# Kernel optimization log

Measured on AMD Instinct MI355X. Metric: run time of the kernel, lower is better.

Reference implementation:

```python
import jax, jax.numpy as jnp
import numpy as np

B, C, H, W = 32, 256, 64, 64
h, w = 8, 8          # partition size
S = 4                # num_sharesets
RED = 4              # globalperceptron_reduce
EPS = 1e-5           # BatchNorm eps


def setup_inputs() -> dict:
    key = jax.random.key(0)
    ks = jax.random.split(key, 20)
    Ci = C // RED
    def bn_params(i):
        return (1.0 + 0.1 * jax.random.normal(ks[i], (S,), jnp.float32),      # gamma
                0.1 * jax.random.normal(ks[i + 1], (S,), jnp.float32),        # beta
                0.1 * jax.random.normal(ks[i + 2], (S,), jnp.float32),        # running_mean
                jax.random.uniform(ks[i + 3], (S,), jnp.float32, 0.5, 1.5))   # running_var
    g3, b3, m3, v3 = bn_params(6)
    g1, b1, m1, v1 = bn_params(10)
    gk, bk, mk, vk = bn_params(14)
    return {
        "x": jax.random.normal(ks[0], (B, C, H, W), jnp.float32),
        # GlobalPerceptron (1x1 convs on pooled vector == dense layers)
        "fc1_w": 0.05 * jax.random.normal(ks[1], (Ci, C), jnp.float32),
        "fc1_b": jnp.zeros((Ci,), jnp.float32),
        "fc2_w": 0.05 * jax.random.normal(ks[2], (C, Ci), jnp.float32),
        "fc2_b": jnp.zeros((C,), jnp.float32),
        # fc3: grouped 1x1 conv over S*h*w channels -> S independent (h*w,h*w) mats
        "fc3_w": 0.05 * jax.random.normal(ks[3], (S, h * w, h * w), jnp.float32),
        "fc3bn_g": g3, "fc3bn_b": b3, "fc3bn_m": m3, "fc3bn_v": v3,
        # reparam depthwise conv branches (k=1 and k=3), groups=S
        "conv1_w": 0.1 * jax.random.normal(ks[4], (S, 1, 1, 1), jnp.float32),
        "bn1_g": g1, "bn1_b": b1, "bn1_m": m1, "bn1_v": v1,
        "conv3_w": 0.1 * jax.random.normal(ks[5], (S, 1, 3, 3), jnp.float32),
        "bn3_g": gk, "bn3_b": bk, "bn3_m": mk, "bn3_v": vk,
    }


def _bn(x, g, b, m, v):
    # inference-mode BatchNorm2d over channel dim 1 (S channels)
    scale = g / jnp.sqrt(v + EPS)
    return x * scale[None, :, None, None] + (b - m * scale)[None, :, None, None]


def _dwconv(x, wgt, k):
    # depthwise (groups=S) conv, stride 1, SAME-ish padding k//2
    return jax.lax.conv_general_dilated(
        x, wgt, (1, 1), [(k // 2, k // 2)] * 2,
        feature_group_count=S, dimension_numbers=("NCHW", "OIHW", "NCHW"))


def reference(x, fc1_w, fc1_b, fc2_w, fc2_b, fc3_w,
              fc3bn_g, fc3bn_b, fc3bn_m, fc3bn_v,
              conv1_w, bn1_g, bn1_b, bn1_m, bn1_v,
              conv3_w, bn3_g, bn3_b, bn3_m, bn3_v):
    hp, wp = H // h, W // w
    # GlobalPerceptron gate: avgpool -> fc -> relu -> fc -> sigmoid
    pooled = x.mean((2, 3))  # (B, C)
    gate = jax.nn.sigmoid(jnp.maximum(pooled @ fc1_w.T + fc1_b, 0.0) @ fc2_w.T + fc2_b)
    # partition: (B,C,H,W) -> (B,hp,wp,C,h,w)
    parts = x.reshape(B, C, hp, h, wp, w).transpose(0, 2, 4, 1, 3, 5)
    # fc3 grouped 1x1 conv: rows of S consecutive channels' (h*w) patches
    fc_in = parts.reshape(-1, S, h * w)                      # (B*hp*wp*C/S, S, h*w)
    fc3_out = jnp.einsum('nsi,soi->nso', fc_in, fc3_w).reshape(-1, S, h, w)
    fc3_out = _bn(fc3_out, fc3bn_g, fc3bn_b, fc3bn_m, fc3bn_v)
    # multi-branch depthwise convs on the same partitions, summed
    conv_in = parts.reshape(-1, S, h, w)
    conv_out = (_bn(_dwconv(conv_in, conv1_w, 1), bn1_g, bn1_b, bn1_m, bn1_v)
                + _bn(_dwconv(conv_in, conv3_w, 3), bn3_g, bn3_b, bn3_m, bn3_v))
    # merge, un-partition (literal translation of the torch reshape/permute chain)
    out = (fc3_out + conv_out).reshape(-1, hp, wp, S, h, w)
    out = out.transpose(0, 3, 1, 4, 2, 5).reshape(B, C, H, W)
    return out * gate[:, :, None, None]
```

## Files before the change

### kernel.cpp

```cpp
#include <hip/hip_runtime.h>
#include <hip/hip_bf16.h>
#include <math.h>

#define BN_EPS 1e-5f

typedef __attribute__((ext_vector_type(8))) short short8;
typedef __attribute__((ext_vector_type(4))) float f32x4;

__device__ __forceinline__ unsigned short bfbits(float f) {
  __hip_bfloat16 h = __float2bfloat16(f);
  return *reinterpret_cast<unsigned short*>(&h);
}
__device__ __forceinline__ float bf2f(unsigned short u) {
  union { unsigned v; float f; } c; c.v = ((unsigned)u) << 16;
  return c.f;
}

__global__ __launch_bounds__(256) void prep_kernel(
    const float* __restrict__ fc3_w,
    const float* __restrict__ g3, const float* __restrict__ b3,
    const float* __restrict__ m3, const float* __restrict__ v3,
    const float* __restrict__ c1w,
    const float* __restrict__ g1, const float* __restrict__ b1,
    const float* __restrict__ m1, const float* __restrict__ v1,
    const float* __restrict__ c3w,
    const float* __restrict__ gk, const float* __restrict__ bk,
    const float* __restrict__ mk, const float* __restrict__ vk,
    unsigned short* __restrict__ ahi, unsigned short* __restrict__ alo,
    float* __restrict__ totb) {
  int blk = blockIdx.x;
  int s = blk >> 2;
  int t = threadIdx.x;
  int o = (blk & 3) * 16 + (t >> 4);
  int kc = (t & 15) * 4;
  float sc3 = g3[s] * rsqrtf(v3[s] + BN_EPS);
  float sc1 = g1[s] * rsqrtf(v1[s] + BN_EPS);
  float sck = gk[s] * rsqrtf(vk[s] + BN_EPS);
  float c0 = sc1 * c1w[s] + sck * c3w[s * 9 + 4];
  int oh = o >> 3, ow = o & 7;
  unsigned short H[4], L[4];
#pragma unroll
  for (int j = 0; j < 4; ++j) {
    int k = kc + j;
    int kh = k >> 3, kw = k & 7;
    float a = sc3 * fc3_w[(s * 64 + o) * 64 + k];
    int dy = kh - oh, dx = kw - ow;
    if (dy >= -1 && dy <= 1 && dx >= -1 && dx <= 1)
      a += (dy == 0 && dx == 0) ? c0 : sck * c3w[s * 9 + (dy + 1) * 3 + (dx + 1)];
    unsigned short h = bfbits(a);
    H[j] = h;
    L[j] = bfbits(a - bf2f(h));
  }
  size_t base = (size_t)(s * 64 + o) * 64 + kc;
  *(ushort4*)(ahi + base) = make_ushort4(H[0], H[1], H[2], H[3]);
  *(ushort4*)(alo + base) = make_ushort4(L[0], L[1], L[2], L[3]);
  if (blk == 0 && t < 4) {
    int ss = t;
    float s3 = g3[ss] * rsqrtf(v3[ss] + BN_EPS);
    float s1 = g1[ss] * rsqrtf(v1[ss] + BN_EPS);
    float sk = gk[ss] * rsqrtf(vk[ss] + BN_EPS);
    totb[ss] = (b3[ss] - m3[ss] * s3) + (b1[ss] - m1[ss] * s1) + (bk[ss] - mk[ss] * sk);
  }
}

__global__ __launch_bounds__(256) void pool_kernel(const float* __restrict__ x,
                                                   float* __restrict__ pooled) {
  int bc = blockIdx.x;
  const float4* xp = reinterpret_cast<const float4*>(x + (size_t)bc * 4096);
  int tid = threadIdx.x;
  float s = 0.f;
#pragma unroll
  for (int k = 0; k < 4; ++k) {
    float4 v = xp[k * 256 + tid];
    s += (v.x + v.y) + (v.z + v.w);
  }
#pragma unroll
  for (int m = 32; m >= 1; m >>= 1) s += __shfl_xor(s, m, 64);
  __shared__ float wsum[4];
  if ((tid & 63) == 0) wsum[tid >> 6] = s;
  __syncthreads();
  if (tid == 0) pooled[bc] = (wsum[0] + wsum[1] + wsum[2] + wsum[3]) * (1.f / 4096.f);
}

__global__ __launch_bounds__(256) void gate_kernel(const float* __restrict__ pooled,
                                                   const float* __restrict__ fc1_w,
                                                   const float* __restrict__ fc1_b,
                                                   const float* __restrict__ fc2_w,
                                                   const float* __restrict__ fc2_b,
                                                   float* __restrict__ gate) {
  int b = blockIdx.x;
  int tid = threadIdx.x;
  __shared__ float p[256];
  __shared__ float hbuf[64];
  p[tid] = pooled[b * 256 + tid];
  __syncthreads();
  if (tid < 64) {
    float a = fc1_b[tid];
    const float* wr = fc1_w + tid * 256;
#pragma unroll 8
    for (int c = 0; c < 256; ++c) a += p[c] * wr[c];
    hbuf[tid] = fmaxf(a, 0.f);
  }
  __syncthreads();
  float g = fc2_b[tid];
  const float* w2 = fc2_w + tid * 64;
#pragma unroll 8
  for (int j = 0; j < 64; ++j) g += hbuf[j] * w2[j];
  gate[b * 256 + tid] = 1.f / (1.f + expf(-g));
}

__global__ __launch_bounds__(256, 3) void main_kernel(
    const float* __restrict__ x,
    const unsigned short* __restrict__ ahi, const unsigned short* __restrict__ alo,
    const float* __restrict__ totb, const float* __restrict__ gate,
    float* __restrict__ out) {
  int bid = blockIdx.x;
  int cgh = bid & 7;
  int hpi = (bid >> 3) & 7;
  int b   = bid >> 6;
  int tid = threadIdx.x;
  int s   = __builtin_amdgcn_readfirstlane(tid >> 6);
  int r16 = tid & 15;
  int g   = (tid >> 4) & 3;

  float tb = totb[s];

  short8 Ah[2][4], Al[2][4];
#pragma unroll
  for (int ot = 0; ot < 4; ++ot)
#pragma unroll
    for (int kt = 0; kt < 2; ++kt) {
      size_t off = (size_t)(s * 64 + ot * 16 + r16) * 64 + kt * 32 + g * 8;
      Ah[kt][ot] = *(const short8*)(ahi + off);
      Al[kt][ot] = *(const short8*)(alo + off);
    }

  f32x4 acc[4][4];
#pragma unroll
  for (int i = 0; i < 4; ++i)
#pragma unroll
    for (int j = 0; j < 4; ++j) acc[i][j] = f32x4{0.f, 0.f, 0.f, 0.f};

#pragma unroll
  for (int kt = 0; kt < 2; ++kt)
#pragma unroll
    for (int nt = 0; nt < 4; ++nt) {
      int n2 = nt * 16 + r16;
      int c_in = (cgh * 8 + (n2 & 7)) * 4 + s;
      const float* bp = x + (size_t)(b * 256 + c_in) * 4096
                        + (hpi * 8 + kt * 4 + g) * 64 + (n2 >> 3) * 8;
      float4 f0 = *(const float4*)bp;
      float4 f1 = *(const float4*)(bp + 4);
      float fv[8] = {f0.x, f0.y, f0.z, f0.w, f1.x, f1.y, f1.z, f1.w};
      union { unsigned short u[8]; short8 v; } BH, BL;
#pragma unroll
      for (int j = 0; j < 8; ++j) {
        unsigned short h = bfbits(fv[j]);
        BH.u[j] = h;
        BL.u[j] = bfbits(fv[j] - bf2f(h));
      }
#pragma unroll
      for (int ot = 0; ot < 4; ++ot) {
        acc[ot][nt] = __builtin_amdgcn_mfma_f32_16x16x32_bf16(Ah[kt][ot], BH.v, acc[ot][nt], 0, 0, 0);
        acc[ot][nt] = __builtin_amdgcn_mfma_f32_16x16x32_bf16(Ah[kt][ot], BL.v, acc[ot][nt], 0, 0, 0);
        acc[ot][nt] = __builtin_amdgcn_mfma_f32_16x16x32_bf16(Al[kt][ot], BH.v, acc[ot][nt], 0, 0, 0);
      }
    }

#pragma unroll
  for (int nt = 0; nt < 4; ++nt) {
    int n2 = nt * 16 + r16;
    int c_out = hpi * 32 + (n2 >> 3) * 4 + s;
    float gmul = gate[b * 256 + c_out];
    float* outb = out + (size_t)(b * 256 + c_out) * 4096 + cgh * 8 * 64 + (n2 & 7) * 8;
#pragma unroll
    for (int ot = 0; ot < 4; ++ot) {
      f32x4 a = acc[ot][nt];
      int hh = ot * 2 + (g >> 1);
      int wo = (g & 1) * 4;
      f32x4 o4 = {(a.x + tb) * gmul, (a.y + tb) * gmul,
                  (a.z + tb) * gmul, (a.w + tb) * gmul};
      __builtin_nontemporal_store(o4, (f32x4*)(outb + hh * 64 + wo));
    }
  }
}

extern "C" void kernel_launch(void* const* d_in, const int* in_sizes, int n_in,
                              void* d_out, int out_size, void* d_ws, size_t ws_size,
                              hipStream_t stream) {
  const float* x     = (const float*)d_in[0];
  const float* fc1_w = (const float*)d_in[1];
  const float* fc1_b = (const float*)d_in[2];
  const float* fc2_w = (const float*)d_in[3];
  const float* fc2_b = (const float*)d_in[4];
  const float* fc3_w = (const float*)d_in[5];
  const float* g3  = (const float*)d_in[6];
  const float* b3  = (const float*)d_in[7];
  const float* m3  = (const float*)d_in[8];
  const float* v3  = (const float*)d_in[9];
  const float* c1w = (const float*)d_in[10];
  const float* g1  = (const float*)d_in[11];
  const float* b1  = (const float*)d_in[12];
  const float* m1  = (const float*)d_in[13];
  const float* v1  = (const float*)d_in[14];
  const float* c3w = (const float*)d_in[15];
  const float* gk  = (const float*)d_in[16];
  const float* bk  = (const float*)d_in[17];
  const float* mk  = (const float*)d_in[18];
  const float* vk  = (const float*)d_in[19];
  float* out = (float*)d_out;

  float* pooled = (float*)d_ws;
  float* gate   = pooled + 8192;
  unsigned short* ahi = (unsigned short*)(gate + 8192);
  unsigned short* alo = ahi + 16384;
  float* totb   = (float*)(alo + 16384);

  prep_kernel<<<16, 256, 0, stream>>>(fc3_w, g3, b3, m3, v3, c1w,
                                      g1, b1, m1, v1, c3w, gk, bk, mk, vk,
                                      ahi, alo, totb);
  pool_kernel<<<8192, 256, 0, stream>>>(x, pooled);
  gate_kernel<<<32, 256, 0, stream>>>(pooled, fc1_w, fc1_b, fc2_w, fc2_b, gate);
  main_kernel<<<2048, 256, 0, stream>>>(x, ahi, alo, totb, gate, out);
}
```

Baseline: 85.06 us.

## Merge prep into pool kernel and split main kernel work across more blocks

```diff
diff --git a/kernel.cpp b/kernel.cpp
--- a/kernel.cpp
+++ b/kernel.cpp
@@ -16,7 +16,8 @@
   return c.f;
 }
 
-__global__ __launch_bounds__(256) void prep_kernel(
+__global__ __launch_bounds__(256) void prep_pool_kernel(
+    const float* __restrict__ x, float* __restrict__ pooled,
     const float* __restrict__ fc3_w,
     const float* __restrict__ g3, const float* __restrict__ b3,
     const float* __restrict__ m3, const float* __restrict__ v3,
@@ -28,46 +29,44 @@
     const float* __restrict__ mk, const float* __restrict__ vk,
     unsigned short* __restrict__ ahi, unsigned short* __restrict__ alo,
     float* __restrict__ totb) {
-  int blk = blockIdx.x;
-  int s = blk >> 2;
-  int t = threadIdx.x;
-  int o = (blk & 3) * 16 + (t >> 4);
-  int kc = (t & 15) * 4;
-  float sc3 = g3[s] * rsqrtf(v3[s] + BN_EPS);
-  float sc1 = g1[s] * rsqrtf(v1[s] + BN_EPS);
-  float sck = gk[s] * rsqrtf(vk[s] + BN_EPS);
-  float c0 = sc1 * c1w[s] + sck * c3w[s * 9 + 4];
-  int oh = o >> 3, ow = o & 7;
-  unsigned short H[4], L[4];
-#pragma unroll
-  for (int j = 0; j < 4; ++j) {
-    int k = kc + j;
-    int kh = k >> 3, kw = k & 7;
-    float a = sc3 * fc3_w[(s * 64 + o) * 64 + k];
-    int dy = kh - oh, dx = kw - ow;
-    if (dy >= -1 && dy <= 1 && dx >= -1 && dx <= 1)
-      a += (dy == 0 && dx == 0) ? c0 : sck * c3w[s * 9 + (dy + 1) * 3 + (dx + 1)];
-    unsigned short h = bfbits(a);
-    H[j] = h;
-    L[j] = bfbits(a - bf2f(h));
-  }
-  size_t base = (size_t)(s * 64 + o) * 64 + kc;
-  *(ushort4*)(ahi + base) = make_ushort4(H[0], H[1], H[2], H[3]);
-  *(ushort4*)(alo + base) = make_ushort4(L[0], L[1], L[2], L[3]);
-  if (blk == 0 && t < 4) {
-    int ss = t;
-    float s3 = g3[ss] * rsqrtf(v3[ss] + BN_EPS);
-    float s1 = g1[ss] * rsqrtf(v1[ss] + BN_EPS);
-    float sk = gk[ss] * rsqrtf(vk[ss] + BN_EPS);
-    totb[ss] = (b3[ss] - m3[ss] * s3) + (b1[ss] - m1[ss] * s1) + (bk[ss] - mk[ss] * sk);
-  }
-}
-
-__global__ __launch_bounds__(256) void pool_kernel(const float* __restrict__ x,
-                                                   float* __restrict__ pooled) {
-  int bc = blockIdx.x;
+  int bid = blockIdx.x;
+  int tid = threadIdx.x;
+  if (bid < 16) {
+    int s = bid >> 2;
+    int o = (bid & 3) * 16 + (tid >> 4);
+    int kc = (tid & 15) * 4;
+    float sc3 = g3[s] * rsqrtf(v3[s] + BN_EPS);
+    float sc1 = g1[s] * rsqrtf(v1[s] + BN_EPS);
+    float sck = gk[s] * rsqrtf(vk[s] + BN_EPS);
+    float c0 = sc1 * c1w[s] + sck * c3w[s * 9 + 4];
+    int oh = o >> 3, ow = o & 7;
+    unsigned short H[4], L[4];
+#pragma unroll
+    for (int j = 0; j < 4; ++j) {
+      int k = kc + j;
+      int kh = k >> 3, kw = k & 7;
+      float a = sc3 * fc3_w[(s * 64 + o) * 64 + k];
+      int dy = kh - oh, dx = kw - ow;
+      if (dy >= -1 && dy <= 1 && dx >= -1 && dx <= 1)
+        a += (dy == 0 && dx == 0) ? c0 : sck * c3w[s * 9 + (dy + 1) * 3 + (dx + 1)];
+      unsigned short h = bfbits(a);
+      H[j] = h;
+      L[j] = bfbits(a - bf2f(h));
+    }
+    size_t base = (size_t)(s * 64 + o) * 64 + kc;
+    *(ushort4*)(ahi + base) = make_ushort4(H[0], H[1], H[2], H[3]);
+    *(ushort4*)(alo + base) = make_ushort4(L[0], L[1], L[2], L[3]);
+    if (bid == 0 && tid < 4) {
+      int ss = tid;
+      float s3 = g3[ss] * rsqrtf(v3[ss] + BN_EPS);
+      float s1 = g1[ss] * rsqrtf(v1[ss] + BN_EPS);
+      float sk = gk[ss] * rsqrtf(vk[ss] + BN_EPS);
+      totb[ss] = (b3[ss] - m3[ss] * s3) + (b1[ss] - m1[ss] * s1) + (bk[ss] - mk[ss] * sk);
+    }
+    return;
+  }
+  int bc = bid - 16;
   const float4* xp = reinterpret_cast<const float4*>(x + (size_t)bc * 4096);
-  int tid = threadIdx.x;
   float s = 0.f;
 #pragma unroll
   for (int k = 0; k < 4; ++k) {
@@ -109,49 +108,56 @@
   gate[b * 256 + tid] = 1.f / (1.f + expf(-g));
 }
 
-__global__ __launch_bounds__(256, 3) void main_kernel(
+__global__ __launch_bounds__(256, 4) void main_kernel(
     const float* __restrict__ x,
     const unsigned short* __restrict__ ahi, const unsigned short* __restrict__ alo,
     const float* __restrict__ totb, const float* __restrict__ gate,
     float* __restrict__ out) {
   int bid = blockIdx.x;
-  int cgh = bid & 7;
-  int hpi = (bid >> 3) & 7;
-  int b   = bid >> 6;
+  int sp  = bid & 1;
+  int cgh = (bid >> 1) & 7;
+  int hpi = (bid >> 4) & 7;
+  int b   = bid >> 7;
   int tid = threadIdx.x;
-  int s   = __builtin_amdgcn_readfirstlane(tid >> 6);
+  int s    = __builtin_amdgcn_readfirstlane(sp * 2 + ((tid >> 7) & 1));
+  int half = __builtin_amdgcn_readfirstlane((tid >> 6) & 1);
   int r16 = tid & 15;
   int g   = (tid >> 4) & 3;
 
   float tb = totb[s];
 
-  short8 Ah[2][4], Al[2][4];
-#pragma unroll
-  for (int ot = 0; ot < 4; ++ot)
+  short8 Ah[2][2], Al[2][2];
+#pragma unroll
+  for (int oti = 0; oti < 2; ++oti)
 #pragma unroll
     for (int kt = 0; kt < 2; ++kt) {
-      size_t off = (size_t)(s * 64 + ot * 16 + r16) * 64 + kt * 32 + g * 8;
-      Ah[kt][ot] = *(const short8*)(ahi + off);
-      Al[kt][ot] = *(const short8*)(alo + off);
-    }
-
-  f32x4 acc[4][4];
-#pragma unroll
-  for (int i = 0; i < 4; ++i)
+      size_t off = (size_t)(s * 64 + (half * 2 + oti) * 16 + r16) * 64 + kt * 32 + g * 8;
+      Ah[kt][oti] = *(const short8*)(ahi + off);
+      Al[kt][oti] = *(const short8*)(alo + off);
+    }
+
+  f32x4 acc[2][4];
+#pragma unroll
+  for (int i = 0; i < 2; ++i)
 #pragma unroll
     for (int j = 0; j < 4; ++j) acc[i][j] = f32x4{0.f, 0.f, 0.f, 0.f};
 
 #pragma unroll
-  for (int kt = 0; kt < 2; ++kt)
+  for (int kt = 0; kt < 2; ++kt) {
+    f32x4 q0[4], q1[4];
 #pragma unroll
     for (int nt = 0; nt < 4; ++nt) {
       int n2 = nt * 16 + r16;
       int c_in = (cgh * 8 + (n2 & 7)) * 4 + s;
       const float* bp = x + (size_t)(b * 256 + c_in) * 4096
                         + (hpi * 8 + kt * 4 + g) * 64 + (n2 >> 3) * 8;
-      float4 f0 = *(const float4*)bp;
-      float4 f1 = *(const float4*)(bp + 4);
-      float fv[8] = {f0.x, f0.y, f0.z, f0.w, f1.x, f1.y, f1.z, f1.w};
+      q0[nt] = *(const f32x4*)bp;
+      q1[nt] = *(const f32x4*)(bp + 4);
+    }
+#pragma unroll
+    for (int nt = 0; nt < 4; ++nt) {
+      float fv[8] = {q0[nt].x, q0[nt].y, q0[nt].z, q0[nt].w,
+                     q1[nt].x, q1[nt].y, q1[nt].z, q1[nt].w};
       union { unsigned short u[8]; short8 v; } BH, BL;
 #pragma unroll
       for (int j = 0; j < 8; ++j) {
@@ -160,12 +166,13 @@
         BL.u[j] = bfbits(fv[j] - bf2f(h));
       }
 #pragma unroll
-      for (int ot = 0; ot < 4; ++ot) {
-        acc[ot][nt] = __builtin_amdgcn_mfma_f32_16x16x32_bf16(Ah[kt][ot], BH.v, acc[ot][nt], 0, 0, 0);
-        acc[ot][nt] = __builtin_amdgcn_mfma_f32_16x16x32_bf16(Ah[kt][ot], BL.v, acc[ot][nt], 0, 0, 0);
-        acc[ot][nt] = __builtin_amdgcn_mfma_f32_16x16x32_bf16(Al[kt][ot], BH.v, acc[ot][nt], 0, 0, 0);
+      for (int oti = 0; oti < 2; ++oti) {
+        acc[oti][nt] = __builtin_amdgcn_mfma_f32_16x16x32_bf16(Ah[kt][oti], BH.v, acc[oti][nt], 0, 0, 0);
+        acc[oti][nt] = __builtin_amdgcn_mfma_f32_16x16x32_bf16(Ah[kt][oti], BL.v, acc[oti][nt], 0, 0, 0);
+        acc[oti][nt] = __builtin_amdgcn_mfma_f32_16x16x32_bf16(Al[kt][oti], BH.v, acc[oti][nt], 0, 0, 0);
       }
     }
+  }
 
 #pragma unroll
   for (int nt = 0; nt < 4; ++nt) {
@@ -174,9 +181,9 @@
     float gmul = gate[b * 256 + c_out];
     float* outb = out + (size_t)(b * 256 + c_out) * 4096 + cgh * 8 * 64 + (n2 & 7) * 8;
 #pragma unroll
-    for (int ot = 0; ot < 4; ++ot) {
-      f32x4 a = acc[ot][nt];
-      int hh = ot * 2 + (g >> 1);
+    for (int oti = 0; oti < 2; ++oti) {
+      f32x4 a = acc[oti][nt];
+      int hh = (half * 2 + oti) * 2 + (g >> 1);
       int wo = (g & 1) * 4;
       f32x4 o4 = {(a.x + tb) * gmul, (a.y + tb) * gmul,
                   (a.z + tb) * gmul, (a.w + tb) * gmul};
@@ -216,10 +223,9 @@
   unsigned short* alo = ahi + 16384;
   float* totb   = (float*)(alo + 16384);
 
-  prep_kernel<<<16, 256, 0, stream>>>(fc3_w, g3, b3, m3, v3, c1w,
-                                      g1, b1, m1, v1, c3w, gk, bk, mk, vk,
-                                      ahi, alo, totb);
-  pool_kernel<<<8192, 256, 0, stream>>>(x, pooled);
+  prep_pool_kernel<<<8208, 256, 0, stream>>>(x, pooled, fc3_w, g3, b3, m3, v3,
+                                             c1w, g1, b1, m1, v1, c3w, gk, bk,
+                                             mk, vk, ahi, alo, totb);
   gate_kernel<<<32, 256, 0, stream>>>(pooled, fc1_w, fc1_b, fc2_w, fc2_b, gate);
-  main_kernel<<<2048, 256, 0, stream>>>(x, ahi, alo, totb, gate, out);
-}
+  main_kernel<<<4096, 256, 0, stream>>>(x, ahi, alo, totb, gate, out);
+}
```

After: 87.42 us. +2.8%, slower.
